# Kernel tuning notes

Hardware: AMD Instinct MI355X
Metric: run time of the kernel (lower is better)

## Reference

```python
import jax, jax.numpy as jnp
import numpy as np

B, N, S, H, W, DG = 16, 64, 4, 32, 32, 8  # batch, base width, scales, spatial, deform groups (=num_cls)
K = 9  # 3x3 kernel
EPS = 1e-5


def conv2d(x, w, b):
    # x: (B,Cin,H,W), w: (Cout,Cin,3,3), stride 1, pad 1
    y = jax.lax.conv_general_dilated(x, w, (1, 1), ((1, 1), (1, 1)),
                                     dimension_numbers=('NCHW', 'OIHW', 'NCHW'))
    return y + b[None, :, None, None]


def bn(x, g, be):
    # BatchNorm2d in training mode: batch stats over (N,H,W) per channel
    m = x.mean(axis=(0, 2, 3), keepdims=True)
    v = x.var(axis=(0, 2, 3), keepdims=True)
    return g[None, :, None, None] * (x - m) / jnp.sqrt(v + EPS) + be[None, :, None, None]


def maxpool(x):
    b, c, h, w = x.shape
    return x.reshape(b, c, h // 2, 2, w // 2, 2).max(axis=(3, 5))


def deform_conv(x, offset, w, b, dg):
    # DCNv1: x (B,Cin,H,W), offset (B,2*K*dg,H,W) laid out as [dg,k,(y,x)], w (Cout,Cin,3,3)
    Bn, Cin, Hh, Ww = x.shape
    Cp = Cin // dg
    off = offset.reshape(Bn, dg, K, 2, Hh, Ww)
    ky = (jnp.arange(K) // 3 - 1).astype(x.dtype)
    kx = (jnp.arange(K) % 3 - 1).astype(x.dtype)
    py = jnp.arange(Hh, dtype=x.dtype)[None, None, None, :, None] + ky[None, None, :, None, None] + off[:, :, :, 0]
    px = jnp.arange(Ww, dtype=x.dtype)[None, None, None, None, :] + kx[None, None, :, None, None] + off[:, :, :, 1]
    y0 = jnp.floor(py)
    x0 = jnp.floor(px)
    ly = py - y0  # (B,dg,K,H,W)
    lx = px - x0
    y0i = y0.astype(jnp.int32)
    x0i = x0.astype(jnp.int32)
    xg = x.reshape(Bn, dg, Cp, Hh * Ww)
    gather = jax.vmap(jax.vmap(lambda f, i: f[:, i]))  # f (Cp,HW), i (K,H,W) -> (Cp,K,H,W)

    def sample(yi, xi):
        valid = (yi >= 0) & (yi < Hh) & (xi >= 0) & (xi < Ww)
        idx = jnp.clip(yi, 0, Hh - 1) * Ww + jnp.clip(xi, 0, Ww - 1)
        vals = gather(xg, idx)  # (B,dg,Cp,K,H,W)
        return vals * valid[:, :, None].astype(x.dtype)

    v00 = sample(y0i, x0i)
    v01 = sample(y0i, x0i + 1)
    v10 = sample(y0i + 1, x0i)
    v11 = sample(y0i + 1, x0i + 1)
    wy = ly[:, :, None]
    wx = lx[:, :, None]
    patches = (v00 * (1 - wy) * (1 - wx) + v01 * (1 - wy) * wx
               + v10 * wy * (1 - wx) + v11 * wy * wx)
    patches = patches.reshape(Bn, Cin, K, Hh, Ww)
    out = jnp.einsum('bckhw,ock->bohw', patches, w.reshape(w.shape[0], Cin, K))
    return out + b[None, :, None, None]


def setup_inputs() -> dict:
    key = jax.random.key(0)
    ks = jax.random.split(key, 24)
    rn = lambda k, shp, s: jax.random.normal(k, shp, dtype=jnp.float32) * s
    inp = {
        'x': rn(ks[0], (B, 3, S, H, W), 1.0),
        'w1': rn(ks[1], (N, 3, 3, 3), float(np.sqrt(2.0 / (9 * 3)))),
        'b1': rn(ks[2], (N,), 0.01),
        'g1': jnp.ones((N,), jnp.float32),
        'be1': jnp.zeros((N,), jnp.float32),
        'w2': rn(ks[3], (2 * N, N, 3, 3), float(np.sqrt(2.0 / (9 * N)))),
        'b2': rn(ks[4], (2 * N,), 0.01),
        'wo1': rn(ks[5], (18 * DG, 2 * N, 3, 3), 0.01),
        'bo1': rn(ks[6], (18 * DG,), 0.01),
        'wd1': rn(ks[7], (2 * N, 2 * N, 3, 3), float(np.sqrt(2.0 / (9 * 2 * N)))),
        'bd1': jnp.ones((2 * N,), jnp.float32),
        'g2': jnp.ones((S,), jnp.float32),
        'be2': jnp.zeros((S,), jnp.float32),
        'wo2': rn(ks[8], (18 * DG, 2 * N, 3, 3), 0.01),
        'bo2': rn(ks[9], (18 * DG,), 0.01),
        'wd2': rn(ks[10], (4 * N, 2 * N, 3, 3), float(np.sqrt(2.0 / (9 * 2 * N)))),
        'bd2': jnp.ones((4 * N,), jnp.float32),
        'g3': jnp.ones((S,), jnp.float32),
        'be3': jnp.zeros((S,), jnp.float32),
        'wfc': rn(ks[11], (10, 4 * N * 64), 0.02),
        'bfc': jnp.zeros((10,), jnp.float32),
    }
    return inp


def reference(x, w1, b1, g1, be1, w2, b2, wo1, bo1, wd1, bd1, g2, be2,
              wo2, bo2, wd2, bd2, g3, be3, wfc, bfc):
    vms = lambda f: jax.vmap(f, in_axes=2, out_axes=2)  # map over scale axis
    h = vms(lambda xi: bn(jax.nn.relu(conv2d(xi, w1, b1)), g1, be1))(x)   # (B,N,S,32,32)
    h = vms(lambda xi: conv2d(xi, w2, b2))(h)                              # (B,2N,S,32,32)
    off1 = vms(lambda xi: conv2d(xi, wo1, bo1))(h)
    h = jnp.stack([deform_conv(h[:, :, i], off1[:, :, i], wd1, bd1, DG)
                   for i in range(S)], axis=2)                             # (B,2N,S,32,32)
    # per-channel BN over scale axis (BatchNorm2d(io_scales)), relu then pool
    h = jax.vmap(lambda xc: maxpool(bn(jax.nn.relu(xc), g2, be2)),
                 in_axes=1, out_axes=1)(h)                                 # (B,2N,S,16,16)
    off2 = vms(lambda xi: conv2d(xi, wo2, bo2))(h)
    h = jnp.stack([deform_conv(h[:, :, i], off2[:, :, i], wd2, bd2, DG)
                   for i in range(S)], axis=2)                             # (B,4N,S,16,16)
    h = jax.vmap(lambda xc: maxpool(bn(xc, g3, be3)),
                 in_axes=1, out_axes=1)(h)                                 # (B,4N,S,8,8)
    embedding = h
    strength = jax.nn.relu(h.max(axis=2))                                  # (B,4N,8,8)
    logits = strength.reshape(strength.shape[0], -1) @ wfc.T + bfc
    return logits, embedding
```

## Files before the change

### kernel.cpp

```cpp
#include <hip/hip_runtime.h>
#include <hip/hip_bf16.h>

#define NIMG 64

typedef __bf16 bf16x8 __attribute__((ext_vector_type(8)));
typedef float f32x4 __attribute__((ext_vector_type(4)));
typedef unsigned int u32x4 __attribute__((ext_vector_type(4)));

__device__ __forceinline__ float bfu2f(ushort u) {
    unsigned v = ((unsigned)u) << 16; float f; __builtin_memcpy(&f, &v, 4); return f;
}
__device__ __forceinline__ ushort f2bfu(float f) {
    __hip_bfloat16 h = __float2bfloat16(f); ushort u; __builtin_memcpy(&u, &h, 2); return u;
}
__device__ __forceinline__ f32x4 mfma16(bf16x8 a, bf16x8 b, f32x4 c) {
    return __builtin_amdgcn_mfma_f32_16x16x32_bf16(a, b, c, 0, 0, 0);
}

__global__ void detect_flag_kernel(const void* __restrict__ g1, int* __restrict__ flag) {
    if (threadIdx.x == 0 && blockIdx.x == 0) {
        unsigned u = *(const unsigned*)g1;
        *flag = (u == 0x3F803F80u) ? 1 : 0;
    }
}

#define NCVT 16
struct CvtDescs { const void* src[NCVT]; float* dst[NCVT]; int n[NCVT]; };
__global__ __launch_bounds__(256) void cvt_batch_kernel(CvtDescs d, const int* __restrict__ flag) {
    const int t = blockIdx.y;
    const int i = blockIdx.x * 256 + threadIdx.x;
    if (i >= d.n[t]) return;
    float v;
    if (*flag) v = bfu2f(((const ushort*)d.src[t])[i]);
    else       v = ((const float*)d.src[t])[i];
    d.dst[t][i] = v;
}

__global__ __launch_bounds__(256) void conv_wt_prep_kernel(const void* __restrict__ src,
                                                           const int* __restrict__ flag,
                                                           ushort* __restrict__ dst, int O, int C) {
    const int i = blockIdx.x * 256 + threadIdx.x;
    if (i >= O * C * 9) return;
    const int kk = i / (O * C);
    const int rem = i - kk * O * C;
    const int o = rem / C, c = rem - o * C;
    const int si = (o * C + c) * 9 + kk;
    dst[i] = (*flag) ? ((const ushort*)src)[si] : f2bfu(((const float*)src)[si]);
}

__global__ __launch_bounds__(256) void deform_wt_frag_kernel(const void* __restrict__ src,
                                                             const int* __restrict__ flag,
                                                             ushort* __restrict__ dst, int O) {
    const int i = blockIdx.x * 256 + threadIdx.x;
    if (i >= O * 1152) return;
    const int j = i & 7;
    const int lane = (i >> 3) & 63;
    const int rem = i >> 9;
    const int chunk = rem % 36;
    const int tile = rem / 36;
    const int n = lane & 15, quad = lane >> 4;
    const int oc = tile * 16 + n;
    const int k = chunk * 32 + quad * 8 + j;
    const int kk = k >> 7, c = k & 127;
    const int si = oc * 1152 + c * 9 + kk;
    dst[i] = (*flag) ? ((const ushort*)src)[si] : f2bfu(((const float*)src)[si]);
}

__global__ __launch_bounds__(256) void conv1_kernel(const float* __restrict__ xf,
                                                    const float* __restrict__ w1,
                                                    const float* __restrict__ b1,
                                                    ushort* __restrict__ h1) {
    __shared__ float wl[1728];
    const int img = blockIdx.x, b = img >> 2, s = img & 3;
    for (int i = threadIdx.x; i < 1728; i += 256) wl[i] = w1[i];
    __syncthreads();
    const int p = blockIdx.y * 256 + threadIdx.x;
    const int y = p >> 5, x = p & 31;
    float v[3][9];
#pragma unroll
    for (int c = 0; c < 3; c++)
#pragma unroll
        for (int dy = 0; dy < 3; dy++)
#pragma unroll
            for (int dx = 0; dx < 3; dx++) {
                const int gy = y + dy - 1, gx = x + dx - 1;
                v[c][dy * 3 + dx] = (gy >= 0 && gy < 32 && gx >= 0 && gx < 32)
                    ? xf[(size_t)(b * 12 + c * 4 + s) * 1024 + gy * 32 + gx] : 0.f;
            }
    ushort* op = h1 + ((size_t)img * 1024 + p) * 64;
#pragma unroll
    for (int og = 0; og < 8; og++) {
        union { u32x4 q; ushort h[8]; } U;
#pragma unroll
        for (int j = 0; j < 8; j++) {
            const int oc = og * 8 + j;
            float acc = b1[oc];
#pragma unroll
            for (int c = 0; c < 3; c++)
#pragma unroll
                for (int k = 0; k < 9; k++) acc = fmaf(v[c][k], wl[(oc * 3 + c) * 9 + k], acc);
            U.h[j] = f2bfu(fmaxf(acc, 0.f));
        }
        *(u32x4*)(op + og * 8) = U.q;
    }
}

__global__ __launch_bounds__(256) void bn1_partial_kernel(const ushort* __restrict__ h1,
                                                          float* __restrict__ pA,
                                                          float* __restrict__ pB) {
    const int bx = blockIdx.x, s = bx & 3, b = bx >> 2;
    const int img = b * 4 + s;
    const int wv = threadIdx.x >> 6, c = threadIdx.x & 63;
    float sum = 0.f, sq = 0.f;
    for (int p = wv * 256; p < wv * 256 + 256; p++) {
        const float v = bfu2f(h1[((size_t)img * 1024 + p) * 64 + c]);
        sum += v; sq = fmaf(v, v, sq);
    }
    const int o = ((s * 16 + b) * 4 + wv) * 64 + c;
    pA[o] = sum; pB[o] = sq;
}
__global__ void bn1_finish_kernel(const float* __restrict__ pA, const float* __restrict__ pB,
                                  const float* __restrict__ g, const float* __restrict__ be,
                                  float* __restrict__ scale, float* __restrict__ shift) {
    const int t = threadIdx.x;
    const int s = t >> 6, c = t & 63;
    float S = 0.f, Q = 0.f;
    for (int bw = 0; bw < 64; bw++) {
        const int o = ((s * 16 + (bw >> 2)) * 4 + (bw & 3)) * 64 + c;
        S += pA[o]; Q += pB[o];
    }
    const float n = 16.f * 1024.f;
    const float mean = S / n;
    const float var = fmaxf(Q / n - mean * mean, 0.f);
    const float inv = rsqrtf(var + 1e-5f);
    const float scv = g[c] * inv;
    scale[t] = scv;
    shift[t] = be[c] - mean * scv;
}

template <int WW, int CIN, int COUT, int OCB, bool AFFINE, bool OUT_NHWC>
__global__ __launch_bounds__(256, 2) void conv_mfma_kernel(
    const ushort* __restrict__ in, const ushort* __restrict__ wt,
    const float* __restrict__ bias, const float* __restrict__ scale,
    const float* __restrict__ shift, ushort* __restrict__ out) {
    constexpr int HW = WW * WW;
    constexpr int TROWS = (WW == 32) ? 8 : 16;
    constexpr int TW = WW + 2;
    constexpr int MT = OCB / 16;
    __shared__ __align__(16) ushort tile[(TROWS + 2) * TW * 32];
    __shared__ __align__(16) ushort wl[9 * OCB * 32];
    const int img = blockIdx.x, s = img & 3;
    const int y0 = blockIdx.y * TROWS;
    const int oc0 = blockIdx.z * OCB;
    const int tid = threadIdx.x;
    const int wv = tid >> 6, lane = tid & 63;
    const int n = lane & 15, quad = lane >> 4;
    f32x4 acc[4][MT];
#pragma unroll
    for (int t = 0; t < 4; t++)
#pragma unroll
        for (int o = 0; o < MT; o++) acc[t][o] = (f32x4){0.f, 0.f, 0.f, 0.f};

    for (int c0 = 0; c0 < CIN; c0 += 32) {
        __syncthreads();
        for (int i = tid; i < (TROWS + 2) * TW * 4; i += 256) {
            const int cg = i & 3, xy = i >> 2;
            const int x = xy % TW, y = xy / TW;
            const int gy = y0 + y - 1, gx = x - 1;
            u32x4 v = {0u, 0u, 0u, 0u};
            if (gy >= 0 && gy < WW && gx >= 0 && gx < WW) {
                v = *(const u32x4*)(in + (size_t)(img * HW + gy * WW + gx) * CIN + c0 + cg * 8);
                if (AFFINE) {
                    union { u32x4 q; ushort h[8]; } U; U.q = v;
#pragma unroll
                    for (int j = 0; j < 8; j++) {
                        const int c = c0 + cg * 8 + j;
                        U.h[j] = f2bfu(fmaf(bfu2f(U.h[j]), scale[s * CIN + c], shift[s * CIN + c]));
                    }
                    v = U.q;
                }
            }
            *(u32x4*)(tile + (y * TW + x) * 32 + cg * 8) = v;
        }
        for (int i = tid; i < 9 * OCB * 4; i += 256) {
            const int cg = i & 3, ko = i >> 2;
            const int oc = ko % OCB, kk = ko / OCB;
            u32x4 v = *(const u32x4*)(wt + (size_t)(kk * COUT + oc0 + oc) * CIN + c0 + cg * 8);
            *(u32x4*)(wl + (kk * OCB + oc) * 32 + cg * 8) = v;
        }
        __syncthreads();
#pragma unroll
        for (int kk = 0; kk < 9; kk++) {
            const int ky = kk / 3, kx = kk % 3;
            bf16x8 bfrag[4];
#pragma unroll
            for (int t = 0; t < 4; t++) {
                const int rt = (WW == 32) ? (2 * wv + (t >> 1)) : (4 * wv + t);
                const int x0 = (WW == 32) ? ((t & 1) * 16) : 0;
                bfrag[t] = *(const bf16x8*)(tile + ((rt + ky) * TW + x0 + n + kx) * 32 + quad * 8);
            }
#pragma unroll
            for (int o = 0; o < MT; o++) {
                const bf16x8 afrag = *(const bf16x8*)(wl + (kk * OCB + o * 16 + n) * 32 + quad * 8);
#pragma unroll
                for (int t = 0; t < 4; t++) acc[t][o] = mfma16(afrag, bfrag[t], acc[t][o]);
            }
        }
    }
#pragma unroll
    for (int t = 0; t < 4; t++) {
        const int rt = (WW == 32) ? (2 * wv + (t >> 1)) : (4 * wv + t);
        const int x0 = (WW == 32) ? ((t & 1) * 16) : 0;
        const int py = y0 + rt, px = x0 + n;
#pragma unroll
        for (int o = 0; o < MT; o++)
#pragma unroll
            for (int r = 0; r < 4; r++) {
                const int oc = oc0 + o * 16 + quad * 4 + r;
                const float v = acc[t][o][r] + bias[oc];
                if (OUT_NHWC) out[(size_t)(img * HW + py * WW + px) * COUT + oc] = f2bfu(v);
                else          out[((size_t)img * COUT + oc) * HW + py * WW + px] = f2bfu(v);
            }
    }
}

template <int COUT, int HH, int WW>
__global__ __launch_bounds__(256, 2) void deform_mfma_kernel(
    const ushort* __restrict__ in, const ushort* __restrict__ off,
    const ushort* __restrict__ wpf, const float* __restrict__ bias,
    ushort* __restrict__ out) {
    constexpr int HW = HH * WW;
    constexpr int PROW = 1160;
    constexpr int NTW = COUT / 32;
    __shared__ __align__(16) ushort Pt[32 * PROW];
    const int img = blockIdx.x;
    const int p0 = blockIdx.y * 32;
    const int tid = threadIdx.x;
    const int wv = tid >> 6, lane = tid & 63;
    const int n = lane & 15, quad = lane >> 4;

    for (int t = tid; t < 32 * 72; t += 256) {
        const int pp = t / 72, r = t - pp * 72;
        const int dg = r & 7, k = r >> 3;
        const int p = p0 + pp;
        const int yy = p / WW, xx = p % WW;
        const float offy = bfu2f(off[((size_t)img * 144 + (dg * 9 + k) * 2 + 0) * HW + p]);
        const float offx = bfu2f(off[((size_t)img * 144 + (dg * 9 + k) * 2 + 1) * HW + p]);
        const float py = (float)(yy + k / 3 - 1) + offy;
        const float px = (float)(xx + k % 3 - 1) + offx;
        const float y0f = floorf(py), x0f = floorf(px);
        const float ly = py - y0f, lx = px - x0f;
        const int iy0 = (int)y0f, ix0 = (int)x0f;
        const int iy1 = iy0 + 1, ix1 = ix0 + 1;
        const bool vy0 = iy0 >= 0 && iy0 < HH, vy1 = iy1 >= 0 && iy1 < HH;
        const bool vx0 = ix0 >= 0 && ix0 < WW, vx1 = ix1 >= 0 && ix1 < WW;
        const int cy0 = min(max(iy0, 0), HH - 1), cy1 = min(max(iy1, 0), HH - 1);
        const int cx0 = min(max(ix0, 0), WW - 1), cx1 = min(max(ix1, 0), WW - 1);
        const float w00 = (1.f - ly) * (1.f - lx) * ((vy0 && vx0) ? 1.f : 0.f);
        const float w01 = (1.f - ly) * lx * ((vy0 && vx1) ? 1.f : 0.f);
        const float w10 = ly * (1.f - lx) * ((vy1 && vx0) ? 1.f : 0.f);
        const float w11 = ly * lx * ((vy1 && vx1) ? 1.f : 0.f);
        const ushort* b00 = in + (size_t)(img * HW + cy0 * WW + cx0) * 128 + dg * 16;
        const ushort* b01 = in + (size_t)(img * HW + cy0 * WW + cx1) * 128 + dg * 16;
        const ushort* b10 = in + (size_t)(img * HW + cy1 * WW + cx0) * 128 + dg * 16;
        const ushort* b11 = in + (size_t)(img * HW + cy1 * WW + cx1) * 128 + dg * 16;
        union { u32x4 q[2]; ushort h[16]; } A0, A1, A2, A3, R;
        A0.q[0] = *(const u32x4*)b00; A0.q[1] = *(const u32x4*)(b00 + 8);
        A1.q[0] = *(const u32x4*)b01; A1.q[1] = *(const u32x4*)(b01 + 8);
        A2.q[0] = *(const u32x4*)b10; A2.q[1] = *(const u32x4*)(b10 + 8);
        A3.q[0] = *(const u32x4*)b11; A3.q[1] = *(const u32x4*)(b11 + 8);
#pragma unroll
        for (int cp = 0; cp < 16; cp++) {
            float v = w00 * bfu2f(A0.h[cp]);
            v = fmaf(w01, bfu2f(A1.h[cp]), v);
            v = fmaf(w10, bfu2f(A2.h[cp]), v);
            v = fmaf(w11, bfu2f(A3.h[cp]), v);
            R.h[cp] = f2bfu(v);
        }
        ushort* dst = Pt + pp * PROW + k * 128 + dg * 16;
        *(u32x4*)dst = R.q[0];
        *(u32x4*)(dst + 8) = R.q[1];
    }
    __syncthreads();

    const int ph = wv >> 1, oh = wv & 1;
    f32x4 acc[NTW];
#pragma unroll
    for (int t = 0; t < NTW; t++) acc[t] = (f32x4){0.f, 0.f, 0.f, 0.f};
    const ushort* wbase = wpf + ((size_t)oh * NTW * 36 + 0) * 512 + lane * 8;
    const ushort* prow = Pt + (ph * 16 + n) * PROW + quad * 8;
#pragma unroll 2
    for (int chunk = 0; chunk < 36; chunk++) {
        const bf16x8 afrag = *(const bf16x8*)(prow + chunk * 32);
#pragma unroll
        for (int t = 0; t < NTW; t++) {
            const bf16x8 bfrag = *(const bf16x8*)(wbase + ((size_t)(t * 36 + chunk)) * 512);
            acc[t] = mfma16(afrag, bfrag, acc[t]);
        }
    }
#pragma unroll
    for (int t = 0; t < NTW; t++) {
        const int oc = (oh * NTW + t) * 16 + n;
        const float bv = bias[oc];
        union { uint2 q; ushort h[4]; } U;
#pragma unroll
        for (int r = 0; r < 4; r++) U.h[r] = f2bfu(acc[t][r] + bv);
        *(uint2*)(out + ((size_t)img * COUT + oc) * HW + p0 + ph * 16 + quad * 4) = U.q;
    }
}

__global__ __launch_bounds__(256) void bn_stats_plane_kernel(
    const ushort* __restrict__ in, int C, int HW, int relu_in,
    const float* __restrict__ gamma, const float* __restrict__ beta,
    float* __restrict__ scale, float* __restrict__ shift) {
    const int g = blockIdx.x;
    const int s = g / C, c = g % C;
    float sum = 0.f, sq = 0.f;
    for (int b = 0; b < 16; b++) {
        const ushort* p = in + ((size_t)(b * 4 + s) * C + c) * HW;
        for (int i = threadIdx.x; i < HW; i += 256) {
            float v = bfu2f(p[i]);
            if (relu_in) v = fmaxf(v, 0.f);
            sum += v; sq = fmaf(v, v, sq);
        }
    }
    for (int o = 32; o > 0; o >>= 1) {
        sum += __shfl_down(sum, o, 64);
        sq += __shfl_down(sq, o, 64);
    }
    __shared__ float as_[4], aq_[4];
    const int wave = threadIdx.x >> 6, lane = threadIdx.x & 63;
    if (lane == 0) { as_[wave] = sum; aq_[wave] = sq; }
    __syncthreads();
    if (threadIdx.x == 0) {
        const float nn = 16.f * (float)HW;
        const float S_ = as_[0] + as_[1] + as_[2] + as_[3];
        const float Q_ = aq_[0] + aq_[1] + aq_[2] + aq_[3];
        const float mean = S_ / nn;
        const float var = fmaxf(Q_ / nn - mean * mean, 0.f);
        const float inv = rsqrtf(var + 1e-5f);
        const float scv = gamma[s] * inv;
        scale[g] = scv;
        shift[g] = beta[s] - mean * scv;
    }
}

__global__ __launch_bounds__(256) void bn_pool_nhwc_kernel(
    const ushort* __restrict__ in, ushort* __restrict__ out,
    const float* __restrict__ scale, const float* __restrict__ shift) {
    const int idx = blockIdx.x * 256 + threadIdx.x;
    const int c = idx & 127;
    const int p = (idx >> 7) & 255;
    const int img = idx >> 15;
    const int s = img & 3;
    const int oy = p >> 4, ox = p & 15;
    const float sc = scale[s * 128 + c], sh = shift[s * 128 + c];
    const ushort* ip = in + ((size_t)img * 128 + c) * 1024 + (2 * oy) * 32 + 2 * ox;
    float m = -3.4e38f;
#pragma unroll
    for (int dy = 0; dy < 2; dy++)
#pragma unroll
        for (int dx = 0; dx < 2; dx++) {
            float v = fmaxf(bfu2f(ip[dy * 32 + dx]), 0.f);
            m = fmaxf(m, fmaf(v, sc, sh));
        }
    out[((size_t)img * 256 + p) * 128 + c] = f2bfu(m);
}

__global__ __launch_bounds__(256) void bn_pool_embed_kernel(
    const ushort* __restrict__ in, void* __restrict__ out, const int* __restrict__ flag,
    float* __restrict__ p2, const float* __restrict__ scale, const float* __restrict__ shift) {
    const int idx = blockIdx.x * 256 + threadIdx.x;
    const int p = idx & 63;
    const int c = (idx >> 6) & 255;
    const int img = idx >> 14;
    const int b = img >> 2, s = img & 3;
    const int oy = p >> 3, ox = p & 7;
    const float sc = scale[s * 256 + c], sh = shift[s * 256 + c];
    const ushort* ip = in + ((size_t)img * 256 + c) * 256 + (2 * oy) * 16 + 2 * ox;
    float m = fmaxf(fmaf(bfu2f(ip[0]), sc, sh), fmaf(bfu2f(ip[1]), sc, sh));
    m = fmaxf(m, fmaf(bfu2f(ip[16]), sc, sh));
    m = fmaxf(m, fmaf(bfu2f(ip[17]), sc, sh));
    p2[idx] = m;
    const size_t eidx = 160 + (((size_t)(b * 256 + c) * 4 + s) * 64) + p;
    if (*flag) ((ushort*)out)[eidx] = f2bfu(m);
    else       ((float*)out)[eidx] = m;
}

__global__ __launch_bounds__(256) void strength_kernel(const float* __restrict__ p2,
                                                       float* __restrict__ st) {
    const int idx = blockIdx.x * 256 + threadIdx.x;
    const int p = idx & 63;
    const int c = (idx >> 6) & 255;
    const int b = idx >> 14;
    const float* e = p2 + ((size_t)(b * 4) * 256 + c) * 64 + p;
    float m = fmaxf(fmaxf(e[0], e[16384]), fmaxf(e[2 * 16384], e[3 * 16384]));
    st[idx] = fmaxf(m, 0.f);
}

__global__ __launch_bounds__(256) void fc_kernel(const float* __restrict__ st,
                                                 const float* __restrict__ wfc,
                                                 const float* __restrict__ bfc,
                                                 void* __restrict__ out,
                                                 const int* __restrict__ flag) {
    const int b = blockIdx.x / 10, o = blockIdx.x % 10;
    const float* sp = st + (size_t)b * 16384;
    const float* wpp = wfc + (size_t)o * 16384;
    float sum = 0.f;
    for (int i = threadIdx.x; i < 16384; i += 256) sum = fmaf(sp[i], wpp[i], sum);
    for (int off = 32; off > 0; off >>= 1) sum += __shfl_down(sum, off, 64);
    __shared__ float ws4[4];
    const int wave = threadIdx.x >> 6, lane = threadIdx.x & 63;
    if (lane == 0) ws4[wave] = sum;
    __syncthreads();
    if (threadIdx.x == 0) {
        const float r = ws4[0] + ws4[1] + ws4[2] + ws4[3] + bfc[o];
        if (*flag) ((ushort*)out)[b * 10 + o] = f2bfu(r);
        else       ((float*)out)[b * 10 + o] = r;
    }
}

extern "C" void kernel_launch(void* const* d_in, const int* in_sizes, int n_in,
                              void* d_out, int out_size, void* d_ws, size_t ws_size,
                              hipStream_t stream) {
    (void)in_sizes; (void)n_in; (void)out_size; (void)ws_size;
    float* ws = (float*)d_ws;
    ushort* wsh = (ushort*)d_ws;
    int* flagp = (int*)d_ws;

    float* xf   = ws + 16;
    float* w1f  = ws + 196624;
    float* b1f  = ws + 198352;
    float* g1f  = ws + 198416;
    float* be1f = ws + 198480;
    float* b2f  = ws + 198544;
    float* bo1f = ws + 198672;
    float* bd1f = ws + 198816;
    float* bo2f = ws + 198944;
    float* bd2f = ws + 199088;
    float* g2f  = ws + 199344; float* be2f = ws + 199348;
    float* g3f  = ws + 199352; float* be3f = ws + 199356;
    float* wfcf = ws + 199360;
    float* bfcf = ws + 363200;
    float* sc1  = ws + 363216; float* sh1 = ws + 363472;
    float* sc2  = ws + 363728; float* sh2 = ws + 364240;
    float* sc3  = ws + 364752; float* sh3 = ws + 365776;
    float* pA   = ws + 366800;
    float* pB   = ws + 383184;
    ushort* w2t  = wsh + 799136;
    ushort* wo1t = wsh + 872864;
    ushort* wo2t = wsh + 1038752;
    ushort* wd1p = wsh + 1204640;
    ushort* wd2p = wsh + 1352096;
    ushort* h1   = wsh + 1647008;
    ushort* h2   = wsh + 5841312;
    ushort* off1 = wsh + 14229920;
    ushort* d1   = wsh + 23667104;
    ushort* p1   = wsh + 1647008;
    ushort* off2 = wsh + 5841312;
    ushort* d2   = wsh + 14229920;
    float* p2    = ws + 11833552;
    float* strg  = ws + 12882128;

    detect_flag_kernel<<<1, 64, 0, stream>>>(d_in[3], flagp);
    CvtDescs cd;
    const int srcIdx[NCVT] = {0, 1, 2, 3, 4, 6, 8, 10, 11, 12, 14, 16, 17, 18, 19, 20};
    float* dsts[NCVT] = {xf, w1f, b1f, g1f, be1f, b2f, bo1f, bd1f, g2f, be2f,
                         bo2f, bd2f, g3f, be3f, wfcf, bfcf};
    const int ns[NCVT] = {196608, 1728, 64, 64, 64, 128, 144, 128, 4, 4,
                          144, 256, 4, 4, 163840, 10};
    for (int i = 0; i < NCVT; i++) { cd.src[i] = d_in[srcIdx[i]]; cd.dst[i] = dsts[i]; cd.n[i] = ns[i]; }
    cvt_batch_kernel<<<dim3(768, NCVT), 256, 0, stream>>>(cd, flagp);
    conv_wt_prep_kernel<<<288, 256, 0, stream>>>(d_in[5], flagp, w2t, 128, 64);
    conv_wt_prep_kernel<<<648, 256, 0, stream>>>(d_in[7], flagp, wo1t, 144, 128);
    conv_wt_prep_kernel<<<648, 256, 0, stream>>>(d_in[13], flagp, wo2t, 144, 128);
    deform_wt_frag_kernel<<<576, 256, 0, stream>>>(d_in[9], flagp, wd1p, 128);
    deform_wt_frag_kernel<<<1152, 256, 0, stream>>>(d_in[15], flagp, wd2p, 256);

    conv1_kernel<<<dim3(NIMG, 4), 256, 0, stream>>>(xf, w1f, b1f, h1);
    bn1_partial_kernel<<<64, 256, 0, stream>>>(h1, pA, pB);
    bn1_finish_kernel<<<1, 256, 0, stream>>>(pA, pB, g1f, be1f, sc1, sh1);
    conv_mfma_kernel<32, 64, 128, 64, true, true>
        <<<dim3(NIMG, 4, 2), 256, 0, stream>>>(h1, w2t, b2f, sc1, sh1, h2);
    conv_mfma_kernel<32, 128, 144, 48, false, false>
        <<<dim3(NIMG, 4, 3), 256, 0, stream>>>(h2, wo1t, bo1f, nullptr, nullptr, off1);
    deform_mfma_kernel<128, 32, 32><<<dim3(NIMG, 32), 256, 0, stream>>>(h2, off1, wd1p, bd1f, d1);
    bn_stats_plane_kernel<<<512, 256, 0, stream>>>(d1, 128, 1024, 1, g2f, be2f, sc2, sh2);
    bn_pool_nhwc_kernel<<<8192, 256, 0, stream>>>(d1, p1, sc2, sh2);

    conv_mfma_kernel<16, 128, 144, 48, false, false>
        <<<dim3(NIMG, 1, 3), 256, 0, stream>>>(p1, wo2t, bo2f, nullptr, nullptr, off2);
    deform_mfma_kernel<256, 16, 16><<<dim3(NIMG, 8), 256, 0, stream>>>(p1, off2, wd2p, bd2f, d2);
    bn_stats_plane_kernel<<<1024, 256, 0, stream>>>(d2, 256, 256, 0, g3f, be3f, sc3, sh3);
    bn_pool_embed_kernel<<<4096, 256, 0, stream>>>(d2, d_out, flagp, p2, sc3, sh3);

    strength_kernel<<<1024, 256, 0, stream>>>(p2, strg);
    fc_kernel<<<160, 256, 0, stream>>>(strg, wfcf, bfcf, d_out, flagp);
}
```

Measured before the change: 398.4 us.

## Fuse bilinear sampling into MFMA A-fragment, drop LDS patch staging in deform conv

The deformable conv kernel no longer builds a full bilinear-sampled patch tile in shared memory before the MFMA loop. Each lane now samples its own 8-channel A fragment directly from global memory inside the chunk loop and feeds it straight into the MFMA. Blocks now cover 64 pixels and a 128-channel output slice, with launch bounds raised for higher occupancy. This removes the LDS round trip and the barrier, but when the second deform conv splits output channels across blocks the sampling work is repeated per channel tile. Offsets are also reloaded per lane per chunk.

```diff
diff --git a/kernel.cpp b/kernel.cpp
--- a/kernel.cpp
+++ b/kernel.cpp
@@ -224,32 +224,42 @@
     }
 }
 
-template <int COUT, int HH, int WW>
-__global__ __launch_bounds__(256, 2) void deform_mfma_kernel(
+template <int COUT, int OCB, int HH, int WW>
+__global__ __launch_bounds__(256, 4) void deform_direct_kernel(
     const ushort* __restrict__ in, const ushort* __restrict__ off,
     const ushort* __restrict__ wpf, const float* __restrict__ bias,
     ushort* __restrict__ out) {
     constexpr int HW = HH * WW;
-    constexpr int PROW = 1160;
-    constexpr int NTW = COUT / 32;
-    __shared__ __align__(16) ushort Pt[32 * PROW];
+    constexpr int QT = OCB / 16;
     const int img = blockIdx.x;
-    const int p0 = blockIdx.y * 32;
+    const int p0 = blockIdx.y * 64;
+    const int tile0 = blockIdx.z * QT;
     const int tid = threadIdx.x;
     const int wv = tid >> 6, lane = tid & 63;
     const int n = lane & 15, quad = lane >> 4;
-
-    for (int t = tid; t < 32 * 72; t += 256) {
-        const int pp = t / 72, r = t - pp * 72;
-        const int dg = r & 7, k = r >> 3;
-        const int p = p0 + pp;
-        const int yy = p / WW, xx = p % WW;
-        const float offy = bfu2f(off[((size_t)img * 144 + (dg * 9 + k) * 2 + 0) * HW + p]);
-        const float offx = bfu2f(off[((size_t)img * 144 + (dg * 9 + k) * 2 + 1) * HW + p]);
-        const float py = (float)(yy + k / 3 - 1) + offy;
-        const float px = (float)(xx + k % 3 - 1) + offx;
-        const float y0f = floorf(py), x0f = floorf(px);
-        const float ly = py - y0f, lx = px - x0f;
+    const int p = p0 + wv * 16 + n;
+    const int yy = p / WW, xx = p % WW;
+
+    f32x4 acc[QT];
+#pragma unroll
+    for (int t = 0; t < QT; t++) acc[t] = (f32x4){0.f, 0.f, 0.f, 0.f};
+    const ushort* wbase = wpf + ((size_t)tile0 * 36) * 512 + lane * 8;
+    const ushort* ibase = in + (size_t)img * HW * 128;
+    const ushort* obase = off + (size_t)img * 144 * HW + p;
+
+#pragma unroll 2
+    for (int chunk = 0; chunk < 36; chunk++) {
+        const int gk = chunk * 32 + quad * 8;
+        const int kk = gk >> 7;
+        const int dg = (gk & 127) >> 4;
+        const int cp0 = gk & 15;
+        const int ch = dg * 9 + kk;
+        const float offy = bfu2f(obase[(ch * 2 + 0) * HW]);
+        const float offx = bfu2f(obase[(ch * 2 + 1) * HW]);
+        const float py = (float)(yy + kk / 3 - 1) + offy;
+        const float pxf = (float)(xx + kk % 3 - 1) + offx;
+        const float y0f = floorf(py), x0f = floorf(pxf);
+        const float ly = py - y0f, lx = pxf - x0f;
         const int iy0 = (int)y0f, ix0 = (int)x0f;
         const int iy1 = iy0 + 1, ix1 = ix0 + 1;
         const bool vy0 = iy0 >= 0 && iy0 < HH, vy1 = iy1 >= 0 && iy1 < HH;
@@ -260,52 +270,35 @@
         const float w01 = (1.f - ly) * lx * ((vy0 && vx1) ? 1.f : 0.f);
         const float w10 = ly * (1.f - lx) * ((vy1 && vx0) ? 1.f : 0.f);
         const float w11 = ly * lx * ((vy1 && vx1) ? 1.f : 0.f);
-        const ushort* b00 = in + (size_t)(img * HW + cy0 * WW + cx0) * 128 + dg * 16;
-        const ushort* b01 = in + (size_t)(img * HW + cy0 * WW + cx1) * 128 + dg * 16;
-        const ushort* b10 = in + (size_t)(img * HW + cy1 * WW + cx0) * 128 + dg * 16;
-        const ushort* b11 = in + (size_t)(img * HW + cy1 * WW + cx1) * 128 + dg * 16;
-        union { u32x4 q[2]; ushort h[16]; } A0, A1, A2, A3, R;
-        A0.q[0] = *(const u32x4*)b00; A0.q[1] = *(const u32x4*)(b00 + 8);
-        A1.q[0] = *(const u32x4*)b01; A1.q[1] = *(const u32x4*)(b01 + 8);
-        A2.q[0] = *(const u32x4*)b10; A2.q[1] = *(const u32x4*)(b10 + 8);
-        A3.q[0] = *(const u32x4*)b11; A3.q[1] = *(const u32x4*)(b11 + 8);
-#pragma unroll
-        for (int cp = 0; cp < 16; cp++) {
-            float v = w00 * bfu2f(A0.h[cp]);
-            v = fmaf(w01, bfu2f(A1.h[cp]), v);
-            v = fmaf(w10, bfu2f(A2.h[cp]), v);
-            v = fmaf(w11, bfu2f(A3.h[cp]), v);
-            R.h[cp] = f2bfu(v);
-        }
-        ushort* dst = Pt + pp * PROW + k * 128 + dg * 16;
-        *(u32x4*)dst = R.q[0];
-        *(u32x4*)(dst + 8) = R.q[1];
-    }
-    __syncthreads();
-
-    const int ph = wv >> 1, oh = wv & 1;
-    f32x4 acc[NTW];
-#pragma unroll
-    for (int t = 0; t < NTW; t++) acc[t] = (f32x4){0.f, 0.f, 0.f, 0.f};
-    const ushort* wbase = wpf + ((size_t)oh * NTW * 36 + 0) * 512 + lane * 8;
-    const ushort* prow = Pt + (ph * 16 + n) * PROW + quad * 8;
-#pragma unroll 2
-    for (int chunk = 0; chunk < 36; chunk++) {
-        const bf16x8 afrag = *(const bf16x8*)(prow + chunk * 32);
-#pragma unroll
-        for (int t = 0; t < NTW; t++) {
+        const ushort* cbase = ibase + dg * 16 + cp0;
+        union { u32x4 q; ushort h[8]; } A0, A1, A2, A3, R;
+        A0.q = *(const u32x4*)(cbase + (size_t)(cy0 * WW + cx0) * 128);
+        A1.q = *(const u32x4*)(cbase + (size_t)(cy0 * WW + cx1) * 128);
+        A2.q = *(const u32x4*)(cbase + (size_t)(cy1 * WW + cx0) * 128);
+        A3.q = *(const u32x4*)(cbase + (size_t)(cy1 * WW + cx1) * 128);
+#pragma unroll
+        for (int j = 0; j < 8; j++) {
+            float v = w00 * bfu2f(A0.h[j]);
+            v = fmaf(w01, bfu2f(A1.h[j]), v);
+            v = fmaf(w10, bfu2f(A2.h[j]), v);
+            v = fmaf(w11, bfu2f(A3.h[j]), v);
+            R.h[j] = f2bfu(v);
+        }
+        const bf16x8 afrag = *(const bf16x8*)&R;
+#pragma unroll
+        for (int t = 0; t < QT; t++) {
             const bf16x8 bfrag = *(const bf16x8*)(wbase + ((size_t)(t * 36 + chunk)) * 512);
             acc[t] = mfma16(afrag, bfrag, acc[t]);
         }
     }
 #pragma unroll
-    for (int t = 0; t < NTW; t++) {
-        const int oc = (oh * NTW + t) * 16 + n;
+    for (int t = 0; t < QT; t++) {
+        const int oc = (tile0 + t) * 16 + n;
         const float bv = bias[oc];
-        union { uint2 q; ushort h[4]; } U;
-#pragma unroll
-        for (int r = 0; r < 4; r++) U.h[r] = f2bfu(acc[t][r] + bv);
-        *(uint2*)(out + ((size_t)img * COUT + oc) * HW + p0 + ph * 16 + quad * 4) = U.q;
+        union { uint2 q; ushort h4[4]; } U;
+#pragma unroll
+        for (int r = 0; r < 4; r++) U.h4[r] = f2bfu(acc[t][r] + bv);
+        *(uint2*)(out + ((size_t)img * COUT + oc) * HW + p0 + wv * 16 + quad * 4) = U.q;
     }
 }
 
@@ -484,13 +477,15 @@
         <<<dim3(NIMG, 4, 2), 256, 0, stream>>>(h1, w2t, b2f, sc1, sh1, h2);
     conv_mfma_kernel<32, 128, 144, 48, false, false>
         <<<dim3(NIMG, 4, 3), 256, 0, stream>>>(h2, wo1t, bo1f, nullptr, nullptr, off1);
-    deform_mfma_kernel<128, 32, 32><<<dim3(NIMG, 32), 256, 0, stream>>>(h2, off1, wd1p, bd1f, d1);
+    deform_direct_kernel<128, 128, 32, 32>
+        <<<dim3(NIMG, 16, 1), 256, 0, stream>>>(h2, off1, wd1p, bd1f, d1);
     bn_stats_plane_kernel<<<512, 256, 0, stream>>>(d1, 128, 1024, 1, g2f, be2f, sc2, sh2);
     bn_pool_nhwc_kernel<<<8192, 256, 0, stream>>>(d1, p1, sc2, sh2);
 
     conv_mfma_kernel<16, 128, 144, 48, false, false>
         <<<dim3(NIMG, 1, 3), 256, 0, stream>>>(p1, wo2t, bo2f, nullptr, nullptr, off2);
-    deform_mfma_kernel<256, 16, 16><<<dim3(NIMG, 8), 256, 0, stream>>>(p1, off2, wd2p, bd2f, d2);
+    deform_direct_kernel<256, 128, 16, 16>
+        <<<dim3(NIMG, 4, 2), 256, 0, stream>>>(p1, off2, wd2p, bd2f, d2);
     bn_stats_plane_kernel<<<1024, 256, 0, stream>>>(d2, 256, 256, 0, g3f, be3f, sc3, sh3);
     bn_pool_embed_kernel<<<4096, 256, 0, stream>>>(d2, d_out, flagp, p2, sc3, sh3);
 
```

Result: slower. 436.0 us (+9.4%).
